# Performance work log

Measured on AMD Instinct MI355X. Metric: run time of the kernel, lower is better.

The kernel has to match this reference:

```python
import jax, jax.numpy as jnp
import numpy as np

NEG_INF = -1e30  # safe -inf surrogate to avoid nan in logsumexp


def _ctc_loss_sum(log_probs, labels, input_lengths, label_lengths):
    # log_probs: (T, N, C) already log-softmaxed; blank = 0
    T, N, C = log_probs.shape
    S = labels.shape[1]
    L = 2 * S + 1  # extended label sequence: blank-interleaved

    # extended labels: [blank, y1, blank, y2, ..., blank]
    ext = jnp.zeros((N, L), dtype=jnp.int32).at[:, 1::2].set(labels.astype(jnp.int32))
    # gather emission log-probs for extended labels: (T, N, L)
    lp_ext = jnp.take_along_axis(log_probs, jnp.broadcast_to(ext[None], (T, N, L)), axis=2)

    # transition from l-2 allowed only for non-blank labels differing from ext[l-2]
    ext_m2 = jnp.pad(ext, ((0, 0), (2, 0)), constant_values=-1)[:, :L]
    allow_skip = (ext != 0) & (ext != ext_m2)  # (N, L)

    # alpha at t=0
    alpha0 = jnp.full((N, L), NEG_INF, dtype=log_probs.dtype)
    alpha0 = alpha0.at[:, 0].set(lp_ext[0, :, 0])
    alpha0 = alpha0.at[:, 1].set(jnp.where(label_lengths > 0, lp_ext[0, :, 1], NEG_INF))

    def step(alpha, t_and_lp):
        t, lp_t = t_and_lp  # lp_t: (N, L)
        a1 = jnp.pad(alpha, ((0, 0), (1, 0)), constant_values=NEG_INF)[:, :L]
        a2 = jnp.pad(alpha, ((0, 0), (2, 0)), constant_values=NEG_INF)[:, :L]
        a2 = jnp.where(allow_skip, a2, NEG_INF)
        m = jnp.maximum(jnp.maximum(alpha, a1), a2)
        lse = m + jnp.log(jnp.exp(alpha - m) + jnp.exp(a1 - m) + jnp.exp(a2 - m))
        new = jnp.where(m > NEG_INF / 2, lse + lp_t, NEG_INF)
        # freeze alpha past each sequence's input length
        alpha = jnp.where((t < input_lengths)[:, None], new, alpha)
        return alpha, None

    alpha, _ = jax.lax.scan(step, alpha0, (jnp.arange(1, T), lp_ext[1:]))

    # log-likelihood = logsumexp(alpha[2*Sl], alpha[2*Sl - 1])
    idx = (2 * label_lengths).astype(jnp.int32)
    a_last = jnp.take_along_axis(alpha, idx[:, None], axis=1)[:, 0]
    a_prev = jnp.take_along_axis(alpha, jnp.maximum(idx - 1, 0)[:, None], axis=1)[:, 0]
    a_prev = jnp.where(label_lengths > 0, a_prev, NEG_INF)
    m = jnp.maximum(a_last, a_prev)
    ll = m + jnp.log(jnp.exp(a_last - m) + jnp.exp(a_prev - m))
    loss = -ll
    # zero_infinity=True: replace infinite losses with 0
    loss = jnp.where(loss < -NEG_INF / 2, loss, 0.0)
    return jnp.sum(loss)


def setup_inputs() -> dict:
    T, N, C, S = 512, 32, 4000, 64
    key = jax.random.key(0)
    k1, k2 = jax.random.split(key)
    inputs = jax.random.normal(k1, (T, N, C), dtype=jnp.float32)
    labels = jax.random.randint(k2, (N, S), 1, C, dtype=jnp.int32)  # exclude blank=0
    input_lengths = jnp.full((N,), T, dtype=jnp.int32)
    label_lengths = jnp.full((N,), S, dtype=jnp.int32)
    return {"inputs": inputs, "labels": labels,
            "input_lengths": input_lengths, "label_lengths": label_lengths}


def reference(inputs, labels, input_lengths, label_lengths):
    log_probs = jax.nn.log_softmax(inputs, axis=2)
    return _ctc_loss_sum(log_probs, labels, input_lengths, label_lengths)
```

## Files before the change

kernel.cpp:

```cpp
#include <hip/hip_runtime.h>

#define LN2 0.6931471805599453f

constexpr int T = 512, N = 32, C = 4000, S = 64;
constexpr int TN   = T * N;
constexpr int ROWF = 68;
constexpr int CT   = 16;
constexpr int NCF  = 8;
constexpr int NCB  = 24;
constexpr int NCG  = 32;

__global__ __launch_bounds__(256) void k_softmax_probs(
    const float* __restrict__ x, const int* __restrict__ labels,
    float* __restrict__ pp, float* __restrict__ ee)
{
    int row  = blockIdx.x * 4 + (threadIdx.x >> 6);
    int lane = threadIdx.x & 63;
    const float*  rp  = x + (size_t)row * C;
    const float4* rp4 = reinterpret_cast<const float4*>(rp);

    float m = -INFINITY, s = 0.f;
    #pragma unroll
    for (int k = 0; k < 15; ++k) {
        float4 v = rp4[lane + 64 * k];
        float mv = fmaxf(fmaxf(v.x, v.y), fmaxf(v.z, v.w));
        float s4 = __expf(v.x - mv) + __expf(v.y - mv) +
                   __expf(v.z - mv) + __expf(v.w - mv);
        float nm = fmaxf(m, mv);
        s = s * __expf(m - nm) + s4 * __expf(mv - nm);
        m = nm;
    }
    if (lane < 40) {
        float4 v = rp4[960 + lane];
        float mv = fmaxf(fmaxf(v.x, v.y), fmaxf(v.z, v.w));
        float s4 = __expf(v.x - mv) + __expf(v.y - mv) +
                   __expf(v.z - mv) + __expf(v.w - mv);
        float nm = fmaxf(m, mv);
        s = s * __expf(m - nm) + s4 * __expf(mv - nm);
        m = nm;
    }
    for (int off = 32; off; off >>= 1) {
        float om = __shfl_xor(m, off), os = __shfl_xor(s, off);
        float nm = fmaxf(m, om);
        s = s * __expf(m - nm) + os * __expf(om - nm);
        m = nm;
    }
    float logZ = m + __logf(s);

    int t = row >> 5, n = row & 31;
    int c  = labels[n * S + lane];
    float zb = rp[0];
    float zl = rp[c];

    float wm = zl;
    for (int off = 32; off; off >>= 1) wm = fmaxf(wm, __shfl_xor(wm, off));
    wm = fmaxf(wm, zb);
    float pm = __expf(wm - logZ);
    int e = (int)(__float_as_uint(pm) >> 23) - 127;

    float* outp = pp + ((size_t)n * T + t) * ROWF;
    outp[1 + lane] = ldexpf(__expf(zl - logZ), -e);
    if (lane == 0) {
        outp[0] = ldexpf(__expf(zb - logZ), -e);
        ee[n * T + t] = (float)e;
    }
}

__device__ __forceinline__ float dpp_shr1_zero(float x) {
    int r = __builtin_amdgcn_update_dpp(0, __float_as_int(x),
                                        0x138 , 0xf, 0xf, false);
    return __int_as_float(r);
}
__device__ __forceinline__ float dpp_shl1_zero(float x) {
    int r = __builtin_amdgcn_update_dpp(0, __float_as_int(x),
                                        0x130 , 0xf, 0xf, false);
    return __int_as_float(r);
}
template <int CTRL>
__device__ __forceinline__ float dpp_max_step(float x) {
    int t = __builtin_amdgcn_update_dpp(__float_as_int(x), __float_as_int(x),
                                        CTRL, 0xf, 0xf, false);
    return fmaxf(x, __int_as_float(t));
}
__device__ __forceinline__ float wave_max_bcast(float x) {
    x = dpp_max_step<0xB1>(x);  x = dpp_max_step<0x4E>(x);
    x = dpp_max_step<0x141>(x); x = dpp_max_step<0x140>(x);
    x = dpp_max_step<0x142>(x); x = dpp_max_step<0x143>(x);
    return __int_as_float(__builtin_amdgcn_readlane(__float_as_int(x), 63));
}

__global__ __launch_bounds__(128) void k_ctc_alpha(
    const float* __restrict__ pp, const float* __restrict__ ee,
    const int* __restrict__ labels,
    const int* __restrict__ input_len, const int* __restrict__ label_len,
    float* __restrict__ out)
{
    __shared__ __align__(16) float ldsF[2][CT][ROWF];
    __shared__ __align__(16) float ldsB[2][CT][ROWF];
    __shared__ float gj[132];
    const int n = blockIdx.x;
    const int wid = threadIdx.x >> 6, lane = threadIdx.x & 63;
    const int Tin = input_len[n], Sl = label_len[n];
    const float* bp = pp + (size_t)n * T * ROWF;
    const bool hot = (Tin == T);

    const int li   = labels[n * S + lane];
    const int lim1 = lane ? labels[n * S + lane - 1] : -1;
    const float skf  = (lane > 0 && li != 0 && li != lim1) ? 1.f : 0.f;
    const float skUf = dpp_shr1_zero(skf);
    const float skk  = skf * skUf;
    const float skD  = dpp_shl1_zero(skf);
    const float skD2 = dpp_shl1_zero(skD);

    asm volatile("s_waitcnt vmcnt(0)" ::: "memory");
    __builtin_amdgcn_sched_barrier(0);

    float a0 = 0.f, a1 = 0.f, aX = 0.f;
    int SH = 0;

#define ISSUE_F(cc) do {                                                      \
    const float* cp_ = bp + (size_t)(cc) * CT * ROWF;                         \
    if (lane < 17) {                                                          \
        _Pragma("unroll")                                                     \
        for (int d_ = 0; d_ < CT; ++d_)                                       \
            __builtin_amdgcn_global_load_lds(cp_ + (size_t)d_ * ROWF + lane * 4, \
                                             &ldsF[(cc) & 1][d_][0], 16, 0, 0);\
    } } while (0)
#define ISSUE_B(cc) do {                                                      \
    const float* cp_ = bp + (size_t)(496 - 16 * (cc)) * ROWF;                 \
    if (lane < 17) {                                                          \
        _Pragma("unroll")                                                     \
        for (int d_ = 0; d_ < CT; ++d_)                                       \
            __builtin_amdgcn_global_load_lds(cp_ + (size_t)d_ * ROWF + lane * 4, \
                                             &ldsB[(cc) & 1][d_][0], 16, 0, 0);\
    } } while (0)

#define PAIRS(B, D) do {                                                      \
    const float* R0_ = &ldsF[B][D][0];                                        \
    const float* R1_ = &ldsF[B][(D) + 1][0];                                  \
    float cb1 = R0_[0], cl1 = R0_[1 + lane];                                  \
    float cb2 = R1_[0], cl2 = R1_[1 + lane];                                  \
    float clU = dpp_shr1_zero(cl1);                                           \
    float W   = clU * cl2;                                                    \
    float A   = cb1 * cb2;                                                    \
    float B_  = clU * cb2;                                                    \
    float Cc  = A + B_;                                                       \
    float D_  = skUf * B_;                                                    \
    float s1  = cb1 + cl1;                                                    \
    float E   = s1 * cl2;                                                     \
    float F   = cl1 * cl2;                                                    \
    float G   = skf * W;                                                      \
    float H   = fmaf(skf, F + W, cb1 * cl2);                                  \
    float I   = skk * W;                                                      \
    float Y0  = cl1 * cb2;                                                    \
    float Y1  = s1 * cb2;                                                     \
    float Y2  = skf * Y0;                                                     \
    float p1  = dpp_shr1_zero(a1);                                            \
    float p0  = dpp_shr1_zero(a0);                                            \
    float p2  = dpp_shr1_zero(p1);                                            \
    float n0  = fmaf(p0, B_, a0 * A) + fmaf(p2, D_, p1 * Cc);                 \
    float n1  = fmaf(a1, F, a0 * E) + fmaf(p2, I, fmaf(p1, H, p0 * G));       \
    float nX  = fmaf(a1, Y1, aX * A) + fmaf(p1, Y2, a0 * Y0);                 \
    a0 = n0; a1 = n1; aX = nX;                                                \
} while (0)

#define WINDOW4(B, D0) do {                                                   \
    a0 = ldexpf(a0, kA); a1 = ldexpf(a1, kA); aX = ldexpf(aX, kA);            \
    SH += kA;                                                                 \
    float gnow_ = fmaxf(fmaxf(a0, a1), aX);                                   \
    PAIRS(B, D0);                                                             \
    gs = dpp_max_step<0xB1>(gs);  gs = dpp_max_step<0x4E>(gs);                \
    PAIRS(B, (D0) + 2);                                                       \
    gs = dpp_max_step<0x141>(gs); gs = dpp_max_step<0x140>(gs);               \
    PAIRS(B, (D0) + 4);                                                       \
    gs = dpp_max_step<0x142>(gs); gs = dpp_max_step<0x143>(gs);               \
    PAIRS(B, (D0) + 6);                                                       \
    {   unsigned b_ = (unsigned)__builtin_amdgcn_readlane(__float_as_int(gs), 63); \
        int e_ = (int)(b_ >> 23) - 127;                                       \
        kA = (b_ == 0u) ? 0 : (105 - e_ - kA);                                \
    }                                                                         \
    gs = gnow_;                                                               \
} while (0)

#define CPAIR(B, D) do {                                                      \
    const float* Ru_ = &ldsB[B][D][0];                                        \
    const float* Rv_ = &ldsB[B][(D) + 1][0];                                  \
    float ub_ = Ru_[0], ul_ = Ru_[1 + lane];                                  \
    float vb_ = Rv_[0], vl_ = Rv_[1 + lane];                                  \
    float ulp_ = dpp_shl1_zero(ul_);                                          \
    float vlp_ = dpp_shl1_zero(vl_);                                          \
    float vlpp_ = dpp_shl1_zero(vlp_);                                        \
    float A2_  = ub_ * vb_;                                                   \
    float uv_  = ul_ * vl_;                                                   \
    float c00_ = vl_ * (ub_ + ul_);                                           \
    float c01_ = ul_ * vb_;                                                   \
    float c02_ = (ul_ * skD) * vlp_;                                          \
    float d01_ = (ul_ + ub_) * vb_;                                           \
    float d02_ = vlp_ * fmaf(skD, ul_ + ulp_, ub_);                           \
    float d03_ = (skD * vb_) * ulp_;                                          \
    float d04_ = ((skD * skD2) * ulp_) * vlpp_;                               \
    float g0n1s_ = dpp_shl1_zero(g0);                                         \
    float g0n1_ = (lane == 63) ? gX : g0n1s_;                                 \
    float g1n1_ = dpp_shl1_zero(g1);                                          \
    float g0n2_ = dpp_shl1_zero(g0n1_);                     \
    float g1n2_ = dpp_shl1_zero(g1n1_);                                       \
    float n0_ = fmaf(g0, A2_, g1 * c00_) + fmaf(g0n1_, c01_, g1n1_ * c02_);   \
    float n1_ = fmaf(g1, uv_, g0n1_ * d01_) +                                 \
                fmaf(g1n1_, d02_, fmaf(g0n2_, d03_, g1n2_ * d04_));           \
    float nX_ = A2_ * gX;                                                     \
    g0 = n0_; g1 = n1_; gX = nX_;                                             \
} while (0)

#define BWINC(B, D0) do {                                                     \
    g0 = ldexpf(g0, kB); g1 = ldexpf(g1, kB); gX = ldexpf(gX, kB);            \
    SHb += kB;                                                                \
    float gnow_ = fmaxf(fmaxf(g0, g1), gX);                                   \
    CPAIR(B, (D0) + 6);                                                       \
    gsb = dpp_max_step<0xB1>(gsb);  gsb = dpp_max_step<0x4E>(gsb);            \
    CPAIR(B, (D0) + 4);                                                       \
    gsb = dpp_max_step<0x141>(gsb); gsb = dpp_max_step<0x140>(gsb);           \
    CPAIR(B, (D0) + 2);                                                       \
    gsb = dpp_max_step<0x142>(gsb); gsb = dpp_max_step<0x143>(gsb);           \
    CPAIR(B, (D0));                                                           \
    {   unsigned b_ = (unsigned)__builtin_amdgcn_readlane(__float_as_int(gsb), 63); \
        int e_ = (int)(b_ >> 23) - 127;                                       \
        kB = (b_ == 0u) ? 0 : (90 - e_ - kB);                                 \
    }                                                                         \
    gsb = gnow_;                                                              \
} while (0)

    if (wid == 0) {
        if (hot) {
            int kA = 0; float gs = 0.f;
            ISSUE_F(0); ISSUE_F(1);
            asm volatile("s_waitcnt vmcnt(16)" ::: "memory");
            __builtin_amdgcn_sched_barrier(0);
            a0 = (lane == 0) ? ldsF[0][0][0] : 0.f;
            a1 = (lane == 0 && Sl > 0) ? ldsF[0][0][1] : 0.f;
            {
                float cb = ldsF[0][1][0], cl = ldsF[0][1][1 + lane];
                float p1 = dpp_shr1_zero(a1);
                float n0 = (a0 + p1) * cb;
                float n1 = fmaf(skf, p1, a0 + a1) * cl;
                float nX = (aX + a1) * cb;
                a0 = n0; a1 = n1; aX = nX;
            }
            PAIRS(0, 2); PAIRS(0, 4); PAIRS(0, 6);
            {   float g = wave_max_bcast(fmaxf(fmaxf(a0, a1), aX));
                unsigned b = __float_as_uint(g);
                int k0 = (b == 0u) ? 0 : (105 - ((int)(b >> 23) - 127));
                a0 = ldexpf(a0, k0); a1 = ldexpf(a1, k0); aX = ldexpf(aX, k0);
                SH += k0; kA = 0;
                gs = fmaxf(fmaxf(a0, a1), aX);
            }
            WINDOW4(0, 8);
            __builtin_amdgcn_sched_barrier(0);
            ISSUE_F(2);
            for (int c = 1; c < NCF; ++c) {
                if (c < NCF - 1) { asm volatile("s_waitcnt vmcnt(16)" ::: "memory"); }
                else             { asm volatile("s_waitcnt vmcnt(0)"  ::: "memory"); }
                __builtin_amdgcn_sched_barrier(0);
                int buf = c & 1;
                WINDOW4(buf, 0);
                WINDOW4(buf, 8);
                if (c + 2 < NCF) {
                    __builtin_amdgcn_sched_barrier(0);
                    ISSUE_F(c + 2);
                }
            }
        } else {
#define GSTEP(cc, dd) do {                                                    \
    float cb_ = ldsF[(cc) & 1][dd][0];                                        \
    float cl_ = ldsF[(cc) & 1][dd][1 + lane];                                 \
    float p1_ = dpp_shr1_zero(a1);                                            \
    float na0_ = (a0 + p1_) * cb_;                                            \
    float na1_ = fmaf(skf, p1_, a0 + a1) * cl_;                               \
    float naX_ = (aX + a1) * cb_;                                             \
    int t_ = (cc) * CT + (dd);                                                \
    bool act_ = (unsigned)(t_ - 1) < (unsigned)(Tin - 1);                     \
    a0 = act_ ? na0_ : a0;                                                    \
    a1 = act_ ? na1_ : a1;                                                    \
    aX = act_ ? naX_ : aX;                                                    \
    if (((dd) & 3) == 3) {                                                    \
        float g_ = wave_max_bcast(fmaxf(a0, fmaxf(a1, aX)));                  \
        unsigned b_ = __float_as_uint(g_);                                    \
        int k_ = (b_ == 0u) ? 0 : (100 - ((int)(b_ >> 23) - 127));            \
        a0 = ldexpf(a0, k_); a1 = ldexpf(a1, k_); aX = ldexpf(aX, k_);        \
        SH += k_;                                                             \
    }                                                                         \
} while (0)
            ISSUE_F(0); ISSUE_F(1);
            asm volatile("s_waitcnt vmcnt(16)" ::: "memory");
            __builtin_amdgcn_sched_barrier(0);
            a0 = (lane == 0) ? ldsF[0][0][0] : 0.f;
            a1 = (lane == 0 && Sl > 0) ? ldsF[0][0][1] : 0.f;
            #pragma unroll
            for (int d = 1; d < CT; ++d) GSTEP(0, d);
            __builtin_amdgcn_sched_barrier(0);
            ISSUE_F(2);
            for (int c = 1; c < NCG; ++c) {
                if (c < NCG - 1) { asm volatile("s_waitcnt vmcnt(16)" ::: "memory"); }
                else             { asm volatile("s_waitcnt vmcnt(0)"  ::: "memory"); }
                __builtin_amdgcn_sched_barrier(0);
                #pragma unroll
                for (int d = 0; d < CT; ++d) GSTEP(c, d);
                if (c + 2 < NCG) {
                    __builtin_amdgcn_sched_barrier(0);
                    ISSUE_F(c + 2);
                }
            }
#undef GSTEP
        }
    } else if (hot) {
        float g0 = (lane == Sl) ? 1.f : 0.f;
        float g1 = (Sl > 0 && lane == Sl - 1) ? 1.f : 0.f;
        float gX = (Sl >= S && lane == 63) ? 1.f : 0.f;
        int SHb = 0, kB = 0;
        float gsb = fmaxf(fmaxf(g0, g1), gX);

        ISSUE_B(0); ISSUE_B(1);
        for (int c = 0; c < NCB; ++c) {
            if (c < NCB - 1) { asm volatile("s_waitcnt vmcnt(16)" ::: "memory"); }
            else             { asm volatile("s_waitcnt vmcnt(0)"  ::: "memory"); }
            __builtin_amdgcn_sched_barrier(0);
            int buf = c & 1;
            BWINC(buf, 8);
            BWINC(buf, 0);
            if (c + 2 < NCB) {
                __builtin_amdgcn_sched_barrier(0);
                ISSUE_B(c + 2);
            }
        }
        gj[2 * lane]     = g0;
        gj[2 * lane + 1] = g1;
        if (lane == 63) {
            gj[128] = gX;
            gj[130] = (float)SHb;
        }
    }

    __syncthreads();
    if (wid != 0) return;

    float se = 0.f;
    #pragma unroll
    for (int j = 0; j < 8; ++j) {
        int idx = lane + 64 * j;
        float ev = ee[n * T + idx];
        se += (idx < Tin) ? ev : 0.f;
    }
    for (int off = 32; off; off >>= 1) se += __shfl_xor(se, off);

    if (hot) {
        double term = (double)a0 * (double)gj[2 * lane]
                    + (double)a1 * (double)gj[2 * lane + 1];
        if (lane == 63) term += (double)aX * (double)gj[128];
        for (int off = 32; off; off >>= 1) term += __shfl_xor(term, off);
        if (lane == 0) {
            double SHb = (double)gj[130];
            double ll2 = log2(term) - (double)SH - SHb + (double)se;
            float loss = (float)(-ll2 * (double)LN2);
            if (!(loss < 5e29f)) loss = 0.f;
            atomicAdd(out, loss);
        }
    } else {
        float a_last = (Sl >= S) ? __shfl(aX, 63) : __shfl(a0, Sl);
        float a_prev_raw = __shfl(a1, (Sl > 0) ? (Sl - 1) : 0);
        float a_prev = (Sl > 0) ? a_prev_raw : 0.f;
        if (lane == 0) {
            float sum  = a_last + a_prev;
            float ll2  = log2f(sum) - (float)SH + se;
            float loss = -ll2 * LN2;
            if (!(loss < 5e29f)) loss = 0.f;
            atomicAdd(out, loss);
        }
    }
#undef BWINC
#undef CPAIR
#undef WINDOW4
#undef PAIRS
#undef ISSUE_F
#undef ISSUE_B
}

extern "C" void kernel_launch(void* const* d_in, const int* in_sizes, int n_in,
                              void* d_out, int out_size, void* d_ws, size_t ws_size,
                              hipStream_t stream) {
    const float* x       = (const float*)d_in[0];
    const int*   labels  = (const int*)d_in[1];
    const int*   in_len  = (const int*)d_in[2];
    const int*   lab_len = (const int*)d_in[3];
    float* out  = (float*)d_out;
    float* pp   = (float*)d_ws;
    float* ee   = pp + (size_t)TN * ROWF + 256;

    hipMemsetAsync(out, 0, sizeof(float), stream);
    k_softmax_probs<<<TN / 4, 256, 0, stream>>>(x, labels, pp, ee);
    k_ctc_alpha<<<N, 128, 0, stream>>>(pp, ee, labels, in_len, lab_len, out);
}
```

Baseline: 87.44 us.

## Overlap backward CTC pass with second half of softmax preprocessing

Softmax preprocessing is split into two launches over halves of the time rows. In the second launch, eight extra blocks run the backward (beta) recursion over the late time steps (256..511) already produced by the first launch, concurrently with the softmax of the early half. The final kernel then resumes the backward pass from the stored state for the remaining 128 steps alongside the forward pass, which shortens the serial critical path. The cost is an extra kernel launch, a global state handoff, and heavier blocks that share CUs with the softmax blocks.

```diff
diff --git a/kernel.cpp b/kernel.cpp
--- a/kernel.cpp
+++ b/kernel.cpp
@@ -7,15 +7,38 @@
 constexpr int ROWF = 68;
 constexpr int CT   = 16;
 constexpr int NCF  = 8;
-constexpr int NCB  = 24;
+constexpr int NCBT = 8;
+constexpr int NCBP = 16;
 constexpr int NCG  = 32;
-
-__global__ __launch_bounds__(256) void k_softmax_probs(
+constexpr int HROWS = 8192;
+
+__device__ __forceinline__ float dpp_shr1_zero(float x) {
+    int r = __builtin_amdgcn_update_dpp(0, __float_as_int(x),
+                                        0x138 , 0xf, 0xf, false);
+    return __int_as_float(r);
+}
+__device__ __forceinline__ float dpp_shl1_zero(float x) {
+    int r = __builtin_amdgcn_update_dpp(0, __float_as_int(x),
+                                        0x130 , 0xf, 0xf, false);
+    return __int_as_float(r);
+}
+template <int CTRL>
+__device__ __forceinline__ float dpp_max_step(float x) {
+    int t = __builtin_amdgcn_update_dpp(__float_as_int(x), __float_as_int(x),
+                                        CTRL, 0xf, 0xf, false);
+    return fmaxf(x, __int_as_float(t));
+}
+__device__ __forceinline__ float wave_max_bcast(float x) {
+    x = dpp_max_step<0xB1>(x);  x = dpp_max_step<0x4E>(x);
+    x = dpp_max_step<0x141>(x); x = dpp_max_step<0x140>(x);
+    x = dpp_max_step<0x142>(x); x = dpp_max_step<0x143>(x);
+    return __int_as_float(__builtin_amdgcn_readlane(__float_as_int(x), 63));
+}
+
+__device__ __forceinline__ void softmax_row(
     const float* __restrict__ x, const int* __restrict__ labels,
-    float* __restrict__ pp, float* __restrict__ ee)
+    float* __restrict__ pp, float* __restrict__ ee, int row, int lane)
 {
-    int row  = blockIdx.x * 4 + (threadIdx.x >> 6);
-    int lane = threadIdx.x & 63;
     const float*  rp  = x + (size_t)row * C;
     const float4* rp4 = reinterpret_cast<const float4*>(rp);
 
@@ -66,41 +89,132 @@
     }
 }
 
-__device__ __forceinline__ float dpp_shr1_zero(float x) {
-    int r = __builtin_amdgcn_update_dpp(0, __float_as_int(x),
-                                        0x138 , 0xf, 0xf, false);
-    return __int_as_float(r);
-}
-__device__ __forceinline__ float dpp_shl1_zero(float x) {
-    int r = __builtin_amdgcn_update_dpp(0, __float_as_int(x),
-                                        0x130 , 0xf, 0xf, false);
-    return __int_as_float(r);
-}
-template <int CTRL>
-__device__ __forceinline__ float dpp_max_step(float x) {
-    int t = __builtin_amdgcn_update_dpp(__float_as_int(x), __float_as_int(x),
-                                        CTRL, 0xf, 0xf, false);
-    return fmaxf(x, __int_as_float(t));
-}
-__device__ __forceinline__ float wave_max_bcast(float x) {
-    x = dpp_max_step<0xB1>(x);  x = dpp_max_step<0x4E>(x);
-    x = dpp_max_step<0x141>(x); x = dpp_max_step<0x140>(x);
-    x = dpp_max_step<0x142>(x); x = dpp_max_step<0x143>(x);
-    return __int_as_float(__builtin_amdgcn_readlane(__float_as_int(x), 63));
-}
-
-__global__ __launch_bounds__(128) void k_ctc_alpha(
+#define CPAIR_BODY(LDSPTR, B, D) do {                                         \
+    const float* Ru_ = LDSPTR(B, D);                                          \
+    const float* Rv_ = LDSPTR(B, (D) + 1);                                    \
+    float ub_ = Ru_[0], ul_ = Ru_[1 + lane];                                  \
+    float vb_ = Rv_[0], vl_ = Rv_[1 + lane];                                  \
+    float ulp_ = dpp_shl1_zero(ul_);                                          \
+    float vlp_ = dpp_shl1_zero(vl_);                                          \
+    float vlpp_ = dpp_shl1_zero(vlp_);                                        \
+    float A2_  = ub_ * vb_;                                                   \
+    float uv_  = ul_ * vl_;                                                   \
+    float c00_ = vl_ * (ub_ + ul_);                                           \
+    float c01_ = ul_ * vb_;                                                   \
+    float c02_ = (ul_ * skD) * vlp_;                                          \
+    float d01_ = (ul_ + ub_) * vb_;                                           \
+    float d02_ = vlp_ * fmaf(skD, ul_ + ulp_, ub_);                           \
+    float d03_ = (skD * vb_) * ulp_;                                          \
+    float d04_ = ((skD * skD2) * ulp_) * vlpp_;                               \
+    float g0n1s_ = dpp_shl1_zero(g0);                                         \
+    float g0n1_ = (lane == 63) ? gX : g0n1s_;                                 \
+    float g1n1_ = dpp_shl1_zero(g1);                                          \
+    float g0n2_ = dpp_shl1_zero(g0n1_);                     \
+    float g1n2_ = dpp_shl1_zero(g1n1_);                                       \
+    float n0_ = fmaf(g0, A2_, g1 * c00_) + fmaf(g0n1_, c01_, g1n1_ * c02_);   \
+    float n1_ = fmaf(g1, uv_, g0n1_ * d01_) +                                 \
+                fmaf(g1n1_, d02_, fmaf(g0n2_, d03_, g1n2_ * d04_));           \
+    float nX_ = A2_ * gX;                                                     \
+    g0 = n0_; g1 = n1_; gX = nX_;                                             \
+} while (0)
+
+#define BWINC_BODY(LDSPTR, B, D0) do {                                        \
+    g0 = ldexpf(g0, kB); g1 = ldexpf(g1, kB); gX = ldexpf(gX, kB);            \
+    SHb += kB;                                                                \
+    float gnow_ = fmaxf(fmaxf(g0, g1), gX);                                   \
+    CPAIR_BODY(LDSPTR, B, (D0) + 6);                                          \
+    gsb = dpp_max_step<0xB1>(gsb);  gsb = dpp_max_step<0x4E>(gsb);            \
+    CPAIR_BODY(LDSPTR, B, (D0) + 4);                                          \
+    gsb = dpp_max_step<0x141>(gsb); gsb = dpp_max_step<0x140>(gsb);           \
+    CPAIR_BODY(LDSPTR, B, (D0) + 2);                                          \
+    gsb = dpp_max_step<0x142>(gsb); gsb = dpp_max_step<0x143>(gsb);           \
+    CPAIR_BODY(LDSPTR, B, (D0));                                              \
+    {   unsigned b_ = (unsigned)__builtin_amdgcn_readlane(__float_as_int(gsb), 63); \
+        int e_ = (int)(b_ >> 23) - 127;                                       \
+        kB = (b_ == 0u) ? 0 : (90 - e_ - kB);                                 \
+    }                                                                         \
+    gsb = gnow_;                                                              \
+} while (0)
+
+__global__ __launch_bounds__(256) void k_phase(
+    const float* __restrict__ x, const int* __restrict__ labels,
+    float* __restrict__ pp, float* __restrict__ ee, float* __restrict__ gst,
+    const int* __restrict__ in_len, const int* __restrict__ lab_len,
+    int hrow0, int dobwd)
+{
+    __shared__ __align__(16) float ldsB[4][2][CT][ROWF];
+    const int wid = threadIdx.x >> 6, lane = threadIdx.x & 63;
+
+    if (blockIdx.x >= 8) {
+        softmax_row(x, labels, pp, ee,
+                    hrow0 + ((int)blockIdx.x - 8) * 4 + wid, lane);
+        return;
+    }
+    if (!dobwd) return;
+    const int n = blockIdx.x * 4 + wid;
+    const int Tin = in_len[n], Sl = lab_len[n];
+    if (Tin != T) return;
+    const float* bp = pp + (size_t)n * T * ROWF;
+
+    const int li = labels[n * S + lane];
+    const float skf = (lane > 0 && li != 0 &&
+                       li != labels[n * S + lane - 1]) ? 1.f : 0.f;
+    const float skD  = dpp_shl1_zero(skf);
+    const float skD2 = dpp_shl1_zero(skD);
+
+    float g0 = (lane == Sl) ? 1.f : 0.f;
+    float g1 = (Sl > 0 && lane == Sl - 1) ? 1.f : 0.f;
+    float gX = (Sl >= S && lane == 63) ? 1.f : 0.f;
+    int SHb = 0, kB = 0;
+    float gsb = fmaxf(fmaxf(g0, g1), gX);
+
+    asm volatile("s_waitcnt vmcnt(0)" ::: "memory");
+    __builtin_amdgcn_sched_barrier(0);
+
+#define LDSP(B, D) (&ldsB[wid][B][D][0])
+#define ISSUEB(cc) do {                                                       \
+    const float* cp_ = bp + (size_t)(496 - 16 * (cc)) * ROWF;                 \
+    if (lane < 17) {                                                          \
+        _Pragma("unroll")                                                     \
+        for (int d_ = 0; d_ < CT; ++d_)                                       \
+            __builtin_amdgcn_global_load_lds(cp_ + (size_t)d_ * ROWF + lane * 4, \
+                                             &ldsB[wid][(cc) & 1][d_][0], 16, 0, 0); \
+    } } while (0)
+
+    ISSUEB(0); ISSUEB(1);
+    for (int c = 0; c < NCBP; ++c) {
+        if (c < NCBP - 1) { asm volatile("s_waitcnt vmcnt(16)" ::: "memory"); }
+        else              { asm volatile("s_waitcnt vmcnt(0)"  ::: "memory"); }
+        __builtin_amdgcn_sched_barrier(0);
+        int buf = c & 1;
+        BWINC_BODY(LDSP, buf, 8);
+        BWINC_BODY(LDSP, buf, 0);
+        if (c + 2 < NCBP) {
+            __builtin_amdgcn_sched_barrier(0);
+            ISSUEB(c + 2);
+        }
+    }
+
+    float* st = gst + n * 136;
+    float2 gv; gv.x = g0; gv.y = g1;
+    *reinterpret_cast<float2*>(&st[2 * lane]) = gv;
+    if (lane == 63) { st[128] = gX; st[129] = (float)SHb; }
+#undef ISSUEB
+#undef LDSP
+}
+
+__global__ __launch_bounds__(128) void k_final(
     const float* __restrict__ pp, const float* __restrict__ ee,
-    const int* __restrict__ labels,
-    const int* __restrict__ input_len, const int* __restrict__ label_len,
+    float* __restrict__ gst, const int* __restrict__ labels,
+    const int* __restrict__ in_len, const int* __restrict__ lab_len,
     float* __restrict__ out)
 {
     __shared__ __align__(16) float ldsF[2][CT][ROWF];
-    __shared__ __align__(16) float ldsB[2][CT][ROWF];
+    __shared__ __align__(16) float ldsT[2][CT][ROWF];
     __shared__ float gj[132];
     const int n = blockIdx.x;
     const int wid = threadIdx.x >> 6, lane = threadIdx.x & 63;
-    const int Tin = input_len[n], Sl = label_len[n];
+    const int Tin = in_len[n], Sl = lab_len[n];
     const float* bp = pp + (size_t)n * T * ROWF;
     const bool hot = (Tin == T);
 
@@ -112,9 +226,6 @@
     const float skD  = dpp_shl1_zero(skf);
     const float skD2 = dpp_shl1_zero(skD);
 
-    asm volatile("s_waitcnt vmcnt(0)" ::: "memory");
-    __builtin_amdgcn_sched_barrier(0);
-
     float a0 = 0.f, a1 = 0.f, aX = 0.f;
     int SH = 0;
 
@@ -124,15 +235,15 @@
         _Pragma("unroll")                                                     \
         for (int d_ = 0; d_ < CT; ++d_)                                       \
             __builtin_amdgcn_global_load_lds(cp_ + (size_t)d_ * ROWF + lane * 4, \
-                                             &ldsF[(cc) & 1][d_][0], 16, 0, 0);\
+                                             &ldsF[(cc) & 1][d_][0], 16, 0, 0); \
     } } while (0)
-#define ISSUE_B(cc) do {                                                      \
-    const float* cp_ = bp + (size_t)(496 - 16 * (cc)) * ROWF;                 \
+#define ISSUE_T(cc) do {                                                      \
+    const float* cp_ = bp + (size_t)(240 - 16 * (cc)) * ROWF;                 \
     if (lane < 17) {                                                          \
         _Pragma("unroll")                                                     \
         for (int d_ = 0; d_ < CT; ++d_)                                       \
             __builtin_amdgcn_global_load_lds(cp_ + (size_t)d_ * ROWF + lane * 4, \
-                                             &ldsB[(cc) & 1][d_][0], 16, 0, 0);\
+                                             &ldsT[(cc) & 1][d_][0], 16, 0, 0); \
     } } while (0)
 
 #define PAIRS(B, D) do {                                                      \
@@ -182,52 +293,10 @@
     gs = gnow_;                                                               \
 } while (0)
 
-#define CPAIR(B, D) do {                                                      \
-    const float* Ru_ = &ldsB[B][D][0];                                        \
-    const float* Rv_ = &ldsB[B][(D) + 1][0];                                  \
-    float ub_ = Ru_[0], ul_ = Ru_[1 + lane];                                  \
-    float vb_ = Rv_[0], vl_ = Rv_[1 + lane];                                  \
-    float ulp_ = dpp_shl1_zero(ul_);                                          \
-    float vlp_ = dpp_shl1_zero(vl_);                                          \
-    float vlpp_ = dpp_shl1_zero(vlp_);                                        \
-    float A2_  = ub_ * vb_;                                                   \
-    float uv_  = ul_ * vl_;                                                   \
-    float c00_ = vl_ * (ub_ + ul_);                                           \
-    float c01_ = ul_ * vb_;                                                   \
-    float c02_ = (ul_ * skD) * vlp_;                                          \
-    float d01_ = (ul_ + ub_) * vb_;                                           \
-    float d02_ = vlp_ * fmaf(skD, ul_ + ulp_, ub_);                           \
-    float d03_ = (skD * vb_) * ulp_;                                          \
-    float d04_ = ((skD * skD2) * ulp_) * vlpp_;                               \
-    float g0n1s_ = dpp_shl1_zero(g0);                                         \
-    float g0n1_ = (lane == 63) ? gX : g0n1s_;                                 \
-    float g1n1_ = dpp_shl1_zero(g1);                                          \
-    float g0n2_ = dpp_shl1_zero(g0n1_);                     \
-    float g1n2_ = dpp_shl1_zero(g1n1_);                                       \
-    float n0_ = fmaf(g0, A2_, g1 * c00_) + fmaf(g0n1_, c01_, g1n1_ * c02_);   \
-    float n1_ = fmaf(g1, uv_, g0n1_ * d01_) +                                 \
-                fmaf(g1n1_, d02_, fmaf(g0n2_, d03_, g1n2_ * d04_));           \
-    float nX_ = A2_ * gX;                                                     \
-    g0 = n0_; g1 = n1_; gX = nX_;                                             \
-} while (0)
-
-#define BWINC(B, D0) do {                                                     \
-    g0 = ldexpf(g0, kB); g1 = ldexpf(g1, kB); gX = ldexpf(gX, kB);            \
-    SHb += kB;                                                                \
-    float gnow_ = fmaxf(fmaxf(g0, g1), gX);                                   \
-    CPAIR(B, (D0) + 6);                                                       \
-    gsb = dpp_max_step<0xB1>(gsb);  gsb = dpp_max_step<0x4E>(gsb);            \
-    CPAIR(B, (D0) + 4);                                                       \
-    gsb = dpp_max_step<0x141>(gsb); gsb = dpp_max_step<0x140>(gsb);           \
-    CPAIR(B, (D0) + 2);                                                       \
-    gsb = dpp_max_step<0x142>(gsb); gsb = dpp_max_step<0x143>(gsb);           \
-    CPAIR(B, (D0));                                                           \
-    {   unsigned b_ = (unsigned)__builtin_amdgcn_readlane(__float_as_int(gsb), 63); \
-        int e_ = (int)(b_ >> 23) - 127;                                       \
-        kB = (b_ == 0u) ? 0 : (90 - e_ - kB);                                 \
-    }                                                                         \
-    gsb = gnow_;                                                              \
-} while (0)
+#define LDST(B, D) (&ldsT[B][D][0])
+
+    asm volatile("s_waitcnt vmcnt(0)" ::: "memory");
+    __builtin_amdgcn_sched_barrier(0);
 
     if (wid == 0) {
         if (hot) {
@@ -312,31 +381,29 @@
 #undef GSTEP
         }
     } else if (hot) {
-        float g0 = (lane == Sl) ? 1.f : 0.f;
-        float g1 = (Sl > 0 && lane == Sl - 1) ? 1.f : 0.f;
-        float gX = (Sl >= S && lane == 63) ? 1.f : 0.f;
-        int SHb = 0, kB = 0;
+        float* st = gst + n * 136;
+        float2 g = *reinterpret_cast<const float2*>(&st[2 * lane]);
+        float g0 = g.x, g1 = g.y;
+        float gX = (lane == 63) ? st[128] : 0.f;
+        int SHb = (int)st[129], kB = 0;
         float gsb = fmaxf(fmaxf(g0, g1), gX);
 
-        ISSUE_B(0); ISSUE_B(1);
-        for (int c = 0; c < NCB; ++c) {
-            if (c < NCB - 1) { asm volatile("s_waitcnt vmcnt(16)" ::: "memory"); }
-            else             { asm volatile("s_waitcnt vmcnt(0)"  ::: "memory"); }
+        ISSUE_T(0); ISSUE_T(1);
+        for (int c = 0; c < NCBT; ++c) {
+            if (c < NCBT - 1) { asm volatile("s_waitcnt vmcnt(16)" ::: "memory"); }
+            else              { asm volatile("s_waitcnt vmcnt(0)"  ::: "memory"); }
             __builtin_amdgcn_sched_barrier(0);
             int buf = c & 1;
-            BWINC(buf, 8);
-            BWINC(buf, 0);
-            if (c + 2 < NCB) {
+            BWINC_BODY(LDST, buf, 8);
+            BWINC_BODY(LDST, buf, 0);
+            if (c + 2 < NCBT) {
                 __builtin_amdgcn_sched_barrier(0);
-                ISSUE_B(c + 2);
+                ISSUE_T(c + 2);
             }
         }
         gj[2 * lane]     = g0;
         gj[2 * lane + 1] = g1;
-        if (lane == 63) {
-            gj[128] = gX;
-            gj[130] = (float)SHb;
-        }
+        if (lane == 63) { gj[128] = gX; gj[130] = (float)SHb; }
     }
 
     __syncthreads();
@@ -375,12 +442,11 @@
             atomicAdd(out, loss);
         }
     }
-#undef BWINC
-#undef CPAIR
+#undef LDST
 #undef WINDOW4
 #undef PAIRS
 #undef ISSUE_F
-#undef ISSUE_B
+#undef ISSUE_T
 }
 
 extern "C" void kernel_launch(void* const* d_in, const int* in_sizes, int n_in,
@@ -393,8 +459,13 @@
     float* out  = (float*)d_out;
     float* pp   = (float*)d_ws;
     float* ee   = pp + (size_t)TN * ROWF + 256;
+    float* gst  = ee + TN + 32;
 
     hipMemsetAsync(out, 0, sizeof(float), stream);
-    k_softmax_probs<<<TN / 4, 256, 0, stream>>>(x, labels, pp, ee);
-    k_ctc_alpha<<<N, 128, 0, stream>>>(pp, ee, labels, in_len, lab_len, out);
-}
+    const int NB = 8 + HROWS / 4;
+    k_phase<<<NB, 256, 0, stream>>>(x, labels, pp, ee, gst, in_len, lab_len,
+                                    HROWS, 0);
+    k_phase<<<NB, 256, 0, stream>>>(x, labels, pp, ee, gst, in_len, lab_len,
+                                    0, 1);
+    k_final<<<N, 128, 0, stream>>>(pp, ee, gst, labels, in_len, lab_len, out);
+}
```

After: 77.08 us. -11.8%, faster.
